# Optimization experiments

Measured on AMD Instinct MI355X. Metric: run time of the kernel, lower is better.

## Reference

```python
import jax, jax.numpy as jnp
import numpy as np

B, T, HE, H = 32, 2048, 512, 512


def setup_inputs() -> dict:
    key = jax.random.key(0)
    ks = jax.random.split(key, 10)
    s_e = 1.0 / np.sqrt(HE)
    s_h = 1.0 / np.sqrt(H)
    return {
        "x": jax.random.normal(ks[0], (B, T, HE), dtype=jnp.float32),
        "wu_i": jax.random.normal(ks[1], (HE, H), dtype=jnp.float32) * s_e,
        "wu_h": jax.random.normal(ks[2], (H, H), dtype=jnp.float32) * s_h,
        "bu": jax.random.normal(ks[3], (H,), dtype=jnp.float32) * s_h,
        "wr_i": jax.random.normal(ks[4], (HE, H), dtype=jnp.float32) * s_e,
        "wr_h": jax.random.normal(ks[5], (H, H), dtype=jnp.float32) * s_h,
        "br": jax.random.normal(ks[6], (H,), dtype=jnp.float32) * s_h,
        "wc_i": jax.random.normal(ks[7], (HE, H), dtype=jnp.float32) * s_e,
        "wc_h": jax.random.normal(ks[8], (H, H), dtype=jnp.float32) * s_h,
        "bc": jax.random.normal(ks[9], (H,), dtype=jnp.float32) * s_h,
    }


def reference(x, wu_i, wu_h, bu, wr_i, wr_h, br, wc_i, wc_h, bc):
    # Precompute input projections for all timesteps (one big GEMM each).
    u_in_x = jnp.einsum("bte,eh->bth", x, wu_i) + bu  # (B,T,H)
    r_in_x = jnp.einsum("bte,eh->bth", x, wr_i) + br
    c_in_x = jnp.einsum("bte,eh->bth", x, wc_i) + bc

    h0 = jnp.zeros((x.shape[0], wu_h.shape[0]), dtype=x.dtype)

    def step(h_prev, inputs):
        u_x, r_x, c_x = inputs
        u = jax.nn.sigmoid(u_x + h_prev @ wu_h)
        r = jax.nn.sigmoid(r_x + h_prev @ wr_h)
        # Faithful to source: r * (h_prev @ wc_h) (reset applied after matmul)
        c = jnp.tanh(c_x + r * (h_prev @ wc_h))
        h = (1.0 - u) * h_prev + u * c
        return h, h

    # scan over time: move T to leading axis
    xs = (
        jnp.swapaxes(u_in_x, 0, 1),
        jnp.swapaxes(r_in_x, 0, 1),
        jnp.swapaxes(c_in_x, 0, 1),
    )
    _, ys = jax.lax.scan(step, h0, xs)  # ys: (T,B,H)
    return jnp.swapaxes(ys, 0, 1)  # (B,T,H)
```

## Files before the change

### kernel.cpp

```cpp
#include <hip/hip_runtime.h>
#include <hip/hip_bf16.h>
#include <hip/hip_fp16.h>
#include <stdint.h>

#define BB 32
#define TT 2048
#define HH 512
#define MM (BB*TT)

typedef __attribute__((ext_vector_type(8))) short bf16x8;
typedef __attribute__((ext_vector_type(4))) float f32x4;
typedef __attribute__((ext_vector_type(4))) unsigned short us4;
typedef __attribute__((ext_vector_type(8))) unsigned short us8;
typedef unsigned long long u64;

__device__ __forceinline__ unsigned short f2bf(float f) {
  __hip_bfloat16 h = __float2bfloat16(f);
  return *reinterpret_cast<unsigned short*>(&h);
}
__device__ __forceinline__ float bf2f(unsigned short u) {
  return __uint_as_float(((unsigned int)u) << 16);
}

__device__ __forceinline__ void wg_barrier_lgkm() {
  asm volatile("s_waitcnt lgkmcnt(0)\n\ts_barrier" ::: "memory");
}

__global__ void wconv_kernel(const float* __restrict__ wu, const float* __restrict__ wr,
                             const float* __restrict__ wc,
                             unsigned short* __restrict__ wuT, unsigned short* __restrict__ wrT,
                             unsigned short* __restrict__ wcTh, unsigned short* __restrict__ wcTl) {
  int idx = blockIdx.x * 256 + threadIdx.x;
  int n = idx >> 9, k = idx & 511;
  int src = k * HH + n;
  wuT[idx] = f2bf(wu[src]);
  wrT[idx] = f2bf(wr[src]);
  float v = wc[src];
  unsigned short hi = f2bf(v);
  wcTh[idx] = hi;
  wcTl[idx] = f2bf(v - bf2f(hi));
}

template<int MODE>
__global__ __launch_bounds__(256) void proj_gemm(
    const float* __restrict__ X,
    const unsigned short* __restrict__ B0T,
    const unsigned short* __restrict__ B1T,
    const float* __restrict__ bias0,
    const float* __restrict__ bias1,
    void* __restrict__ outp) {
  __shared__ __attribute__((aligned(16))) unsigned short Ah[128][72];
  __shared__ __attribute__((aligned(16))) unsigned short Al[128][72];
  __shared__ __attribute__((aligned(16))) unsigned short Bs0[64][72];
  __shared__ __attribute__((aligned(16))) unsigned short Bs1[64][72];
  const int tid = threadIdx.x;
  const int w = tid >> 6, l = tid & 63;
  const int lr = l & 15, lk = l >> 4;
  const int rowBase = blockIdx.x * 128;
  const int colBase = blockIdx.y * 64;

  f32x4 acc0[2][4], acc1[2][4];
  const f32x4 zero = {0.f, 0.f, 0.f, 0.f};
  #pragma unroll
  for (int m = 0; m < 2; ++m)
    #pragma unroll
    for (int n = 0; n < 4; ++n) { acc0[m][n] = zero; acc1[m][n] = zero; }

  for (int kt = 0; kt < 8; ++kt) {
    #pragma unroll
    for (int i = 0; i < 8; ++i) {
      int idx = tid + 256 * i;
      int r = idx >> 4, c4 = idx & 15;
      float4 v = *reinterpret_cast<const float4*>(
          X + (size_t)(rowBase + r) * HH + kt * 64 + c4 * 4);
      us4 hv;
      hv.x = f2bf(v.x); hv.y = f2bf(v.y); hv.z = f2bf(v.z); hv.w = f2bf(v.w);
      *reinterpret_cast<us4*>(&Ah[r][c4 * 4]) = hv;
      if (MODE == 1) {
        us4 lv;
        lv.x = f2bf(v.x - bf2f(hv.x)); lv.y = f2bf(v.y - bf2f(hv.y));
        lv.z = f2bf(v.z - bf2f(hv.z)); lv.w = f2bf(v.w - bf2f(hv.w));
        *reinterpret_cast<us4*>(&Al[r][c4 * 4]) = lv;
      }
    }
    #pragma unroll
    for (int i = 0; i < 2; ++i) {
      int idx = tid + 256 * i;
      int n = idx >> 3, k8 = idx & 7;
      const size_t go = (size_t)(colBase + n) * HH + kt * 64 + k8 * 8;
      *reinterpret_cast<us8*>(&Bs0[n][k8 * 8]) = *reinterpret_cast<const us8*>(B0T + go);
      *reinterpret_cast<us8*>(&Bs1[n][k8 * 8]) = *reinterpret_cast<const us8*>(B1T + go);
    }
    __syncthreads();
    #pragma unroll
    for (int ks = 0; ks < 2; ++ks) {
      const int k0 = ks * 32 + lk * 8;
      bf16x8 a[2], b0[4], b1[4];
      #pragma unroll
      for (int m = 0; m < 2; ++m)
        a[m] = *reinterpret_cast<const bf16x8*>(&Ah[32 * w + 16 * m + lr][k0]);
      #pragma unroll
      for (int n = 0; n < 4; ++n) {
        b0[n] = *reinterpret_cast<const bf16x8*>(&Bs0[16 * n + lr][k0]);
        b1[n] = *reinterpret_cast<const bf16x8*>(&Bs1[16 * n + lr][k0]);
      }
      if (MODE == 1) {
        bf16x8 al[2];
        #pragma unroll
        for (int m = 0; m < 2; ++m)
          al[m] = *reinterpret_cast<const bf16x8*>(&Al[32 * w + 16 * m + lr][k0]);
        #pragma unroll
        for (int m = 0; m < 2; ++m)
          #pragma unroll
          for (int n = 0; n < 4; ++n) {
            acc0[m][n] = __builtin_amdgcn_mfma_f32_16x16x32_bf16(a[m],  b0[n], acc0[m][n], 0, 0, 0);
            acc0[m][n] = __builtin_amdgcn_mfma_f32_16x16x32_bf16(a[m],  b1[n], acc0[m][n], 0, 0, 0);
            acc0[m][n] = __builtin_amdgcn_mfma_f32_16x16x32_bf16(al[m], b0[n], acc0[m][n], 0, 0, 0);
          }
      } else {
        #pragma unroll
        for (int m = 0; m < 2; ++m)
          #pragma unroll
          for (int n = 0; n < 4; ++n) {
            acc0[m][n] = __builtin_amdgcn_mfma_f32_16x16x32_bf16(a[m], b0[n], acc0[m][n], 0, 0, 0);
            acc1[m][n] = __builtin_amdgcn_mfma_f32_16x16x32_bf16(a[m], b1[n], acc1[m][n], 0, 0, 0);
          }
      }
    }
    __syncthreads();
  }
  #pragma unroll
  for (int m = 0; m < 2; ++m) {
    #pragma unroll
    for (int n = 0; n < 4; ++n) {
      const int col = colBase + 16 * n + lr;
      const float bv0 = bias0[col];
      const float bv1 = (MODE == 0) ? bias1[col] : 0.f;
      #pragma unroll
      for (int q = 0; q < 4; ++q) {
        const int row = rowBase + 32 * w + 16 * m + lk * 4 + q;
        const size_t o = (size_t)row * HH + col;
        if (MODE == 0) {
          float v0 = acc0[m][n][q] + bv0;
          float v1 = acc1[m][n][q] + bv1;
          unsigned int pk = (unsigned int)__half_as_ushort(__float2half(v0)) |
                            ((unsigned int)__half_as_ushort(__float2half(v1)) << 16);
          reinterpret_cast<unsigned int*>(outp)[o] = pk;
        } else {
          reinterpret_cast<__half*>(outp)[o] = __float2half(acc0[m][n][q] + bv0);
        }
      }
    }
  }
}

__global__ __launch_bounds__(512, 2) void scan_kernel(
    const float* __restrict__ wu_h, const float* __restrict__ wr_h,
    const float* __restrict__ wc_h,
    float* __restrict__ out, const __half* __restrict__ cx,
    u64* __restrict__ hbuf) {
  const int blk = blockIdx.x;
  const int b = (blk & 7) + ((blk >> 6) << 3);
  const int g = (blk >> 3) & 7;
  const int tid = threadIdx.x;
  const int w = tid >> 6, l = tid & 63;
  const int j = g * 64 + l;

  float wu[64], wr[64], wc[64];
  #pragma unroll
  for (int kk = 0; kk < 64; ++kk) {
    const size_t o = (size_t)(w * 64 + kk) * HH + j;
    wu[kk] = wu_h[o]; wr[kk] = wr_h[o]; wc[kk] = wc_h[o];
  }

  __shared__ float parts[8][3][64];
  float hprev = 0.f;
  unsigned int urx_c = 0;
  unsigned short cx_c = 0;
  unsigned int* outu = reinterpret_cast<unsigned int*>(out);
  const unsigned short* cxu = reinterpret_cast<const unsigned short*>(cx);
  const size_t bo = (size_t)b * TT * HH;
  if (w == 0) {
    urx_c = outu[bo + j];
    cx_c = cxu[bo + j];
  }
  u64* const hb_poll = hbuf + (size_t)b * HH + w * 64 + l;
  u64* const hb_own  = hbuf + (size_t)b * HH + j;

  for (int t = 0; t < TT; ++t) {
    float hval = 0.f;
    if (t > 0) {
      u64 v;
      for (;;) {
        v = __hip_atomic_load(hb_poll + (size_t)(t & 1) * (BB * HH),
                              __ATOMIC_RELAXED, __HIP_MEMORY_SCOPE_AGENT);
        if (__all((int)((unsigned int)(v >> 32) >= (unsigned int)t))) break;
      }
      hval = __uint_as_float((unsigned int)v);
    }
    float au = 0.f, ar = 0.f, ac = 0.f;
    const unsigned int hbits = __float_as_uint(hval);
    #pragma unroll
    for (int kk = 0; kk < 64; ++kk) {
      const float hk = __uint_as_float(__builtin_amdgcn_readlane(hbits, kk));
      au = __builtin_fmaf(hk, wu[kk], au);
      ar = __builtin_fmaf(hk, wr[kk], ar);
      ac = __builtin_fmaf(hk, wc[kk], ac);
    }
    parts[w][0][l] = au; parts[w][1][l] = ar; parts[w][2][l] = ac;
    wg_barrier_lgkm();
    if (w == 0) {
      float su = 0.f, sr = 0.f, sc = 0.f;
      #pragma unroll
      for (int ww = 0; ww < 8; ++ww) {
        su += parts[ww][0][l]; sr += parts[ww][1][l]; sc += parts[ww][2][l];
      }
      const float ux = __half2float(__ushort_as_half((unsigned short)(urx_c & 0xffffu)));
      const float rx = __half2float(__ushort_as_half((unsigned short)(urx_c >> 16)));
      const float cxf = __half2float(__ushort_as_half(cx_c));
      const float uu = 1.f / (1.f + __expf(-(su + ux)));
      const float rr = 1.f / (1.f + __expf(-(sr + rx)));
      const float ccv = tanhf(cxf + rr * sc);
      const float h = (1.f - uu) * hprev + uu * ccv;
      hprev = h;
      const u64 pv = ((u64)(unsigned int)(t + 1) << 32) | (u64)__float_as_uint(h);
      __hip_atomic_store(hb_own + (size_t)((t + 1) & 1) * (BB * HH), pv,
                         __ATOMIC_RELAXED, __HIP_MEMORY_SCOPE_AGENT);
      const size_t oidx = bo + (size_t)t * HH + j;
      out[oidx] = h;
      if (t + 1 < TT) {
        urx_c = outu[oidx + HH];
        cx_c = cxu[oidx + HH];
      }
    }
    wg_barrier_lgkm();
  }
}

extern "C" void kernel_launch(void* const* d_in, const int* in_sizes, int n_in,
                              void* d_out, int out_size, void* d_ws, size_t ws_size,
                              hipStream_t stream) {
  const float* x    = (const float*)d_in[0];
  const float* wu_i = (const float*)d_in[1];
  const float* wu_h = (const float*)d_in[2];
  const float* bu   = (const float*)d_in[3];
  const float* wr_i = (const float*)d_in[4];
  const float* wr_h = (const float*)d_in[5];
  const float* br   = (const float*)d_in[6];
  const float* wc_i = (const float*)d_in[7];
  const float* wc_h = (const float*)d_in[8];
  const float* bc   = (const float*)d_in[9];
  float* out = (float*)d_out;

  char* ws = (char*)d_ws;
  __half* cx = (__half*)ws;
  unsigned short* wuT  = (unsigned short*)(ws + (size_t)MM * HH * 2);
  unsigned short* wrT  = wuT + HH * HH;
  unsigned short* wcTh = wrT + HH * HH;
  unsigned short* wcTl = wcTh + HH * HH;
  u64* hbuf = (u64*)(wcTl + HH * HH);

  hipMemsetAsync(hbuf, 0, (size_t)2 * BB * HH * sizeof(u64), stream);
  wconv_kernel<<<1024, 256, 0, stream>>>(wu_i, wr_i, wc_i, wuT, wrT, wcTh, wcTl);
  proj_gemm<0><<<dim3(MM / 128, 8), 256, 0, stream>>>(x, wuT, wrT, bu, br, (void*)out);
  proj_gemm<1><<<dim3(MM / 128, 8), 256, 0, stream>>>(x, wcTh, wcTl, bc, bc, (void*)cx);

  void* args[] = { (void*)&wu_h, (void*)&wr_h, (void*)&wc_h, (void*)&out,
                   (void*)&cx, (void*)&hbuf };
  hipLaunchCooperativeKernel((void*)scan_kernel, dim3(256), dim3(512), args, 0, stream);
}
```

Baseline: 4.508 ms.

## Use LDS atomic accumulation with rotating buffers to drop second barrier per step

The recurrent scan now reduces per-wave partial dot products with LDS atomicAdd into a 4-deep rotating accumulator, so the second workgroup barrier per timestep can be removed. The inner FMA loop uses packed float2 FMAs, and sigmoid and tanh use rcp/exp fast approximations. The aim is to shorten the serial per-step critical path. Correctness of buffer zeroing relies on wave skew staying within the ring depth, and float atomics add nondeterministic summation order.

```diff
diff --git a/kernel.cpp b/kernel.cpp
--- a/kernel.cpp
+++ b/kernel.cpp
@@ -10,6 +10,7 @@
 
 typedef __attribute__((ext_vector_type(8))) short bf16x8;
 typedef __attribute__((ext_vector_type(4))) float f32x4;
+typedef __attribute__((ext_vector_type(2))) float f32x2;
 typedef __attribute__((ext_vector_type(4))) unsigned short us4;
 typedef __attribute__((ext_vector_type(8))) unsigned short us8;
 typedef unsigned long long u64;
@@ -24,6 +25,16 @@
 
 __device__ __forceinline__ void wg_barrier_lgkm() {
   asm volatile("s_waitcnt lgkmcnt(0)\n\ts_barrier" ::: "memory");
+}
+
+__device__ __forceinline__ float fast_sigmoid(float x) {
+  float e = __expf(-x);
+  return __builtin_amdgcn_rcpf(1.f + e);
+}
+__device__ __forceinline__ float fast_tanh(float x) {
+  float xc = fminf(fmaxf(x, -15.f), 15.f);
+  float e2 = __expf(2.f * xc);
+  return (e2 - 1.f) * __builtin_amdgcn_rcpf(e2 + 1.f);
 }
 
 __global__ void wconv_kernel(const float* __restrict__ wu, const float* __restrict__ wr,
@@ -166,14 +177,20 @@
   const int w = tid >> 6, l = tid & 63;
   const int j = g * 64 + l;
 
-  float wu[64], wr[64], wc[64];
+  f32x2 wu2[32], wr2[32], wc2[32];
   #pragma unroll
-  for (int kk = 0; kk < 64; ++kk) {
-    const size_t o = (size_t)(w * 64 + kk) * HH + j;
-    wu[kk] = wu_h[o]; wr[kk] = wr_h[o]; wc[kk] = wc_h[o];
-  }
-
-  __shared__ float parts[8][3][64];
+  for (int i = 0; i < 32; ++i) {
+    const size_t o0 = (size_t)(w * 64 + 2 * i) * HH + j;
+    const size_t o1 = o0 + HH;
+    wu2[i] = f32x2{wu_h[o0], wu_h[o1]};
+    wr2[i] = f32x2{wr_h[o0], wr_h[o1]};
+    wc2[i] = f32x2{wc_h[o0], wc_h[o1]};
+  }
+
+  __shared__ float accum[4][3][64];
+  for (int z = tid; z < 4 * 3 * 64; z += 512) ((float*)accum)[z] = 0.f;
+  __syncthreads();
+
   float hprev = 0.f;
   unsigned int urx_c = 0;
   unsigned short cx_c = 0;
@@ -198,30 +215,37 @@
       }
       hval = __uint_as_float((unsigned int)v);
     }
-    float au = 0.f, ar = 0.f, ac = 0.f;
+    f32x2 au2 = {0.f, 0.f}, ar2 = {0.f, 0.f}, ac2 = {0.f, 0.f};
     const unsigned int hbits = __float_as_uint(hval);
     #pragma unroll
-    for (int kk = 0; kk < 64; ++kk) {
-      const float hk = __uint_as_float(__builtin_amdgcn_readlane(hbits, kk));
-      au = __builtin_fmaf(hk, wu[kk], au);
-      ar = __builtin_fmaf(hk, wr[kk], ar);
-      ac = __builtin_fmaf(hk, wc[kk], ac);
-    }
-    parts[w][0][l] = au; parts[w][1][l] = ar; parts[w][2][l] = ac;
+    for (int i = 0; i < 32; ++i) {
+      f32x2 hp;
+      hp.x = __uint_as_float(__builtin_amdgcn_readlane(hbits, 2 * i));
+      hp.y = __uint_as_float(__builtin_amdgcn_readlane(hbits, 2 * i + 1));
+      au2 = __builtin_elementwise_fma(hp, wu2[i], au2);
+      ar2 = __builtin_elementwise_fma(hp, wr2[i], ar2);
+      ac2 = __builtin_elementwise_fma(hp, wc2[i], ac2);
+    }
+    const int pb = t & 3;
+    atomicAdd(&accum[pb][0][l], au2.x + au2.y);
+    atomicAdd(&accum[pb][1][l], ar2.x + ar2.y);
+    atomicAdd(&accum[pb][2][l], ac2.x + ac2.y);
+    if (w == 1) {
+      const int zb = (t + 2) & 3;
+      accum[zb][0][l] = 0.f; accum[zb][1][l] = 0.f; accum[zb][2][l] = 0.f;
+    }
     wg_barrier_lgkm();
     if (w == 0) {
-      float su = 0.f, sr = 0.f, sc = 0.f;
-      #pragma unroll
-      for (int ww = 0; ww < 8; ++ww) {
-        su += parts[ww][0][l]; sr += parts[ww][1][l]; sc += parts[ww][2][l];
-      }
+      const float su = accum[pb][0][l];
+      const float sr = accum[pb][1][l];
+      const float sc = accum[pb][2][l];
       const float ux = __half2float(__ushort_as_half((unsigned short)(urx_c & 0xffffu)));
       const float rx = __half2float(__ushort_as_half((unsigned short)(urx_c >> 16)));
       const float cxf = __half2float(__ushort_as_half(cx_c));
-      const float uu = 1.f / (1.f + __expf(-(su + ux)));
-      const float rr = 1.f / (1.f + __expf(-(sr + rx)));
-      const float ccv = tanhf(cxf + rr * sc);
-      const float h = (1.f - uu) * hprev + uu * ccv;
+      const float uu = fast_sigmoid(su + ux);
+      const float rr = fast_sigmoid(sr + rx);
+      const float ccv = fast_tanh(cxf + rr * sc);
+      const float h = hprev + uu * (ccv - hprev);
       hprev = h;
       const u64 pv = ((u64)(unsigned int)(t + 1) << 32) | (u64)__float_as_uint(h);
       __hip_atomic_store(hb_own + (size_t)((t + 1) & 1) * (BB * HH), pv,
@@ -233,7 +257,6 @@
         cx_c = cxu[oidx + HH];
       }
     }
-    wg_barrier_lgkm();
   }
 }
 
```

Measured after the change: 6.389 ms. 1.42x slower.
